# Optimization experiments

Measured on AMD Instinct MI355X. Metric: run time of the kernel, lower is better.

## Reference

```python
import jax, jax.numpy as jnp
import numpy as np

EPS = 1e-5  # torch.nn.LayerNorm default

def layernorm(x, gamma, beta):
    mu = jnp.mean(x, axis=-1, keepdims=True)
    var = jnp.mean(jnp.square(x - mu), axis=-1, keepdims=True)
    return (x - mu) * jax.lax.rsqrt(var + EPS) * gamma + beta

def setup_inputs() -> dict:
    key = jax.random.key(0)
    ks = jax.random.split(key, 5)
    B, H = 8192, 1024
    stdv = 1.0 / np.sqrt(H)
    inp = jax.random.normal(ks[0], (B, 4 * H), dtype=jnp.float32)
    hx = jax.random.normal(ks[1], (B, H), dtype=jnp.float32)
    cx = jax.random.normal(ks[2], (B, H), dtype=jnp.float32)
    weight_hh = jax.random.uniform(ks[3], (4 * H, H), dtype=jnp.float32, minval=-stdv, maxval=stdv)
    gamma_h = jnp.ones((4 * H,), jnp.float32)
    beta_h = jnp.zeros((4 * H,), jnp.float32)
    gamma_c = jnp.ones((H,), jnp.float32)
    beta_c = jnp.zeros((H,), jnp.float32)
    return {"input": inp, "hx": hx, "cx": cx, "weight_hh": weight_hh,
            "gamma_h": gamma_h, "beta_h": beta_h, "gamma_c": gamma_c, "beta_c": beta_c}

def reference(input, hx, cx, weight_hh, gamma_h, beta_h, gamma_c, beta_c):
    # hgates = LN(hx @ W_hh^T); gates = igates + hgates
    hgates = layernorm(jnp.matmul(hx, weight_hh.T), gamma_h, beta_h)
    gates = input + hgates  # [B, 4H]
    i_g, f_g, c_g, o_g = jnp.split(gates, 4, axis=1)
    ingate = jax.nn.sigmoid(i_g)
    forgetgate = jax.nn.sigmoid(f_g)
    cellgate = jnp.tanh(c_g)
    outgate = jax.nn.sigmoid(o_g)
    cy = layernorm(forgetgate * cx + ingate * cellgate, gamma_c, beta_c)
    hy = outgate * jnp.tanh(cy)
    return (hy, cy)
```

## Files before the change

### kernel.cpp

```cpp
#include <hip/hip_runtime.h>
#include <hip/hip_bf16.h>

typedef __attribute__((ext_vector_type(8))) short short8;
typedef __attribute__((ext_vector_type(4))) float f32x4;

#define LN_EPS 1e-5f

__device__ __forceinline__ ushort f32_to_bf16(float f) {
  union { float f; unsigned u; } v; v.f = f;
  unsigned u = v.u;
  u += 0x7FFFu + ((u >> 16) & 1u);
  return (ushort)(u >> 16);
}
__device__ __forceinline__ float bf16_to_f32(ushort h) {
  union { unsigned u; float f; } v; v.u = ((unsigned)h) << 16; return v.f;
}
__device__ __forceinline__ float sigmoid_f(float x) {
  return 1.0f / (1.0f + __expf(-x));
}
__device__ __forceinline__ float tanh_f(float x) {
  return 2.0f / (1.0f + __expf(-2.0f * x)) - 1.0f;
}

__global__ __launch_bounds__(256) void cast_f32_bf16(const float* __restrict__ in,
                                                     ushort* __restrict__ out, int n4) {
  int i = blockIdx.x * 256 + threadIdx.x;
  int stride = gridDim.x * 256;
  for (; i < n4; i += stride) {
    float4 v = ((const float4*)in)[i];
    ushort4 o;
    o.x = f32_to_bf16(v.x); o.y = f32_to_bf16(v.y);
    o.z = f32_to_bf16(v.z); o.w = f32_to_bf16(v.w);
    ((ushort4*)out)[i] = o;
  }
}

__global__ __launch_bounds__(256) void gemm_bt(const ushort* __restrict__ A,
                                               const ushort* __restrict__ B,
                                               ushort* __restrict__ C,
                                               int M, int N, int K) {
  __shared__ alignas(16) ushort As[128][40];
  __shared__ alignas(16) ushort Bs[128][40];
  const int tid = threadIdx.x;
  const int lane = tid & 63;
  const int wave = tid >> 6;
  const int wm = wave >> 1, wn = wave & 1;
  const int bn = blockIdx.x, bm = blockIdx.y;

  f32x4 acc[4][4];
#pragma unroll
  for (int i = 0; i < 4; i++)
#pragma unroll
    for (int j = 0; j < 4; j++) acc[i][j] = (f32x4){0.f, 0.f, 0.f, 0.f};

  const int srow = tid >> 2;
  const int scol = (tid & 3) << 3;
  const ushort* Ag = A + (size_t)(bm * 128 + srow) * K + scol;
  const ushort* Bg = B + (size_t)(bn * 128 + srow) * K + scol;
  const int frow = lane & 15;
  const int fcol = (lane >> 4) << 3;

  for (int k0 = 0; k0 < K; k0 += 32) {
    short8 a0 = *(const short8*)(Ag);
    short8 a1 = *(const short8*)(Ag + (size_t)64 * K);
    short8 b0 = *(const short8*)(Bg);
    short8 b1 = *(const short8*)(Bg + (size_t)64 * K);
    __syncthreads();
    *(short8*)&As[srow][scol]      = a0;
    *(short8*)&As[srow + 64][scol] = a1;
    *(short8*)&Bs[srow][scol]      = b0;
    *(short8*)&Bs[srow + 64][scol] = b1;
    __syncthreads();
    Ag += 32; Bg += 32;

    short8 af[4], bfr[4];
#pragma unroll
    for (int i = 0; i < 4; i++) af[i]  = *(const short8*)&As[wm * 64 + i * 16 + frow][fcol];
#pragma unroll
    for (int j = 0; j < 4; j++) bfr[j] = *(const short8*)&Bs[wn * 64 + j * 16 + frow][fcol];
#pragma unroll
    for (int i = 0; i < 4; i++)
#pragma unroll
      for (int j = 0; j < 4; j++)
        acc[i][j] = __builtin_amdgcn_mfma_f32_16x16x32_bf16(af[i], bfr[j], acc[i][j], 0, 0, 0);
  }

  const int crow0 = bm * 128 + wm * 64;
  const int ccol0 = bn * 128 + wn * 64;
#pragma unroll
  for (int i = 0; i < 4; i++)
#pragma unroll
    for (int j = 0; j < 4; j++) {
      int col = ccol0 + j * 16 + (lane & 15);
      int rb = crow0 + i * 16 + ((lane >> 4) << 2);
#pragma unroll
      for (int r = 0; r < 4; r++)
        C[(size_t)(rb + r) * N + col] = f32_to_bf16(acc[i][j][r]);
    }
}

__global__ __launch_bounds__(256) void lstm_ln_kernel(
    const ushort* __restrict__ gates_pre,
    const float* __restrict__ input,
    const float* __restrict__ cx,
    const float* __restrict__ gamma_h, const float* __restrict__ beta_h,
    const float* __restrict__ gamma_c, const float* __restrict__ beta_c,
    float* __restrict__ hy, float* __restrict__ cy, int H) {
  const int FH = 4 * H;
  const int row = blockIdx.x;
  const int t = threadIdx.x;
  const int lane = t & 63, wv = t >> 6;
  __shared__ float gates_s[4096];
  __shared__ float redA[8], redB[8];

  const ushort* gp = gates_pre + (size_t)row * FH;
  const int c0 = t * 8;
  const int c1 = 2048 + t * 8;

  float x[16];
  {
    uint4 u0 = *(const uint4*)(gp + c0);
    uint4 u1 = *(const uint4*)(gp + c1);
    const unsigned* pu0 = (const unsigned*)&u0;
    const unsigned* pu1 = (const unsigned*)&u1;
#pragma unroll
    for (int q = 0; q < 4; q++) {
      x[2 * q]     = bf16_to_f32((ushort)(pu0[q] & 0xFFFFu));
      x[2 * q + 1] = bf16_to_f32((ushort)(pu0[q] >> 16));
      x[8 + 2 * q]     = bf16_to_f32((ushort)(pu1[q] & 0xFFFFu));
      x[8 + 2 * q + 1] = bf16_to_f32((ushort)(pu1[q] >> 16));
    }
  }

  float s1 = 0.f, s2 = 0.f;
#pragma unroll
  for (int q = 0; q < 16; q++) { s1 += x[q]; s2 += x[q] * x[q]; }
  {
    float a = s1, b = s2;
#pragma unroll
    for (int off = 32; off > 0; off >>= 1) {
      a += __shfl_down(a, off, 64);
      b += __shfl_down(b, off, 64);
    }
    if (lane == 0) { redA[wv] = a; redA[4 + wv] = b; }
  }
  __syncthreads();
  const float mu  = (redA[0] + redA[1] + redA[2] + redA[3]) * (1.0f / 4096.f);
  const float m2  = (redA[4] + redA[5] + redA[6] + redA[7]) * (1.0f / 4096.f);
  const float rstd = rsqrtf(m2 - mu * mu + LN_EPS);

  const float* ip = input + (size_t)row * FH;
#pragma unroll
  for (int h = 0; h < 2; h++) {
    const int cc = (h == 0) ? c0 : c1;
    const int xo = h * 8;
    float iv[8], gv[8], bv[8];
    *(float4*)&iv[0] = *(const float4*)(ip + cc);
    *(float4*)&iv[4] = *(const float4*)(ip + cc + 4);
    *(float4*)&gv[0] = *(const float4*)(gamma_h + cc);
    *(float4*)&gv[4] = *(const float4*)(gamma_h + cc + 4);
    *(float4*)&bv[0] = *(const float4*)(beta_h + cc);
    *(float4*)&bv[4] = *(const float4*)(beta_h + cc + 4);
#pragma unroll
    for (int q = 0; q < 8; q++)
      gates_s[cc + q] = (x[xo + q] - mu) * rstd * gv[q] + bv[q] + iv[q];
  }
  __syncthreads();

  const float* cxp = cx + (size_t)row * H;
  float cell[4], og[4];
  float s3 = 0.f, s4 = 0.f;
#pragma unroll
  for (int k = 0; k < 4; k++) {
    const int j = t + 256 * k;
    float ig = gates_s[j];
    float fg = gates_s[H + j];
    float cg = gates_s[2 * H + j];
    float oo = gates_s[3 * H + j];
    float in_s = sigmoid_f(ig);
    float fg_s = sigmoid_f(fg);
    float cg_t = tanh_f(cg);
    og[k] = sigmoid_f(oo);
    float cl = fg_s * cxp[j] + in_s * cg_t;
    cell[k] = cl;
    s3 += cl; s4 += cl * cl;
  }
  {
    float a = s3, b = s4;
#pragma unroll
    for (int off = 32; off > 0; off >>= 1) {
      a += __shfl_down(a, off, 64);
      b += __shfl_down(b, off, 64);
    }
    if (lane == 0) { redB[wv] = a; redB[4 + wv] = b; }
  }
  __syncthreads();
  const float mu2   = (redB[0] + redB[1] + redB[2] + redB[3]) * (1.0f / 1024.f);
  const float m22   = (redB[4] + redB[5] + redB[6] + redB[7]) * (1.0f / 1024.f);
  const float rstd2 = rsqrtf(m22 - mu2 * mu2 + LN_EPS);

#pragma unroll
  for (int k = 0; k < 4; k++) {
    const int j = t + 256 * k;
    float cyv = (cell[k] - mu2) * rstd2 * gamma_c[j] + beta_c[j];
    float hyv = og[k] * tanh_f(cyv);
    cy[(size_t)row * H + j] = cyv;
    hy[(size_t)row * H + j] = hyv;
  }
}

extern "C" void kernel_launch(void* const* d_in, const int* in_sizes, int n_in,
                              void* d_out, int out_size, void* d_ws, size_t ws_size,
                              hipStream_t stream) {
  (void)n_in; (void)out_size; (void)ws_size;
  const float* input   = (const float*)d_in[0];
  const float* hx      = (const float*)d_in[1];
  const float* cx      = (const float*)d_in[2];
  const float* w       = (const float*)d_in[3];
  const float* gamma_h = (const float*)d_in[4];
  const float* beta_h  = (const float*)d_in[5];
  const float* gamma_c = (const float*)d_in[6];
  const float* beta_c  = (const float*)d_in[7];

  const int H  = in_sizes[6];
  const int B  = in_sizes[1] / H;
  const int FH = 4 * H;
  const int K  = H;

  ushort* hx_bf = (ushort*)d_ws;
  ushort* w_bf  = hx_bf + (size_t)B * K;
  ushort* gates = w_bf + (size_t)FH * K;

  float* hy = (float*)d_out;
  float* cy = hy + (size_t)B * H;

  cast_f32_bf16<<<2048, 256, 0, stream>>>(hx, hx_bf, (B * K) / 4);
  cast_f32_bf16<<<1024, 256, 0, stream>>>(w, w_bf, (FH * K) / 4);

  dim3 grid(FH / 128, B / 128);
  gemm_bt<<<grid, 256, 0, stream>>>(hx_bf, w_bf, gates, B, FH, K);

  lstm_ln_kernel<<<B, 256, 0, stream>>>(gates, input, cx, gamma_h, beta_h,
                                        gamma_c, beta_c, hy, cy, H);
}
```

Measured before the change: 382.5 us.

## Use direct global-to-LDS loads with XOR swizzle, merge casts, regularize LSTM epilogue

```diff
diff --git a/kernel.cpp b/kernel.cpp
--- a/kernel.cpp
+++ b/kernel.cpp
@@ -22,16 +22,26 @@
   return 2.0f / (1.0f + __expf(-2.0f * x)) - 1.0f;
 }
 
-__global__ __launch_bounds__(256) void cast_f32_bf16(const float* __restrict__ in,
-                                                     ushort* __restrict__ out, int n4) {
+__device__ __forceinline__ void gload16(const ushort* g, ushort* l) {
+  __builtin_amdgcn_global_load_lds(
+      (const __attribute__((address_space(1))) unsigned int*)g,
+      (__attribute__((address_space(3))) unsigned int*)l, 16, 0, 0);
+}
+
+__global__ __launch_bounds__(256) void cast2_f32_bf16(
+    const float* __restrict__ a, ushort* __restrict__ oa, int na4,
+    const float* __restrict__ b, ushort* __restrict__ ob, int nb4) {
   int i = blockIdx.x * 256 + threadIdx.x;
   int stride = gridDim.x * 256;
-  for (; i < n4; i += stride) {
-    float4 v = ((const float4*)in)[i];
+  for (; i < na4 + nb4; i += stride) {
+    const float* src = (i < na4) ? a : b;
+    ushort* dst = (i < na4) ? oa : ob;
+    int k = (i < na4) ? i : i - na4;
+    float4 v = ((const float4*)src)[k];
     ushort4 o;
     o.x = f32_to_bf16(v.x); o.y = f32_to_bf16(v.y);
     o.z = f32_to_bf16(v.z); o.w = f32_to_bf16(v.w);
-    ((ushort4*)out)[i] = o;
+    ((ushort4*)dst)[k] = o;
   }
 }
 
@@ -39,8 +49,8 @@
                                                const ushort* __restrict__ B,
                                                ushort* __restrict__ C,
                                                int M, int N, int K) {
-  __shared__ alignas(16) ushort As[128][40];
-  __shared__ alignas(16) ushort Bs[128][40];
+  __shared__ alignas(16) ushort As[128 * 32];
+  __shared__ alignas(16) ushort Bs[128 * 32];
   const int tid = threadIdx.x;
   const int lane = tid & 63;
   const int wave = tid >> 6;
@@ -54,30 +64,35 @@
     for (int j = 0; j < 4; j++) acc[i][j] = (f32x4){0.f, 0.f, 0.f, 0.f};
 
   const int srow = tid >> 2;
-  const int scol = (tid & 3) << 3;
-  const ushort* Ag = A + (size_t)(bm * 128 + srow) * K + scol;
-  const ushort* Bg = B + (size_t)(bn * 128 + srow) * K + scol;
+  const int schunk = (tid & 3) ^ ((tid >> 3) & 3);
+  const ushort* Ag = A + (size_t)(bm * 128 + srow) * K + schunk * 8;
+  const ushort* Bg = B + (size_t)(bn * 128 + srow) * K + schunk * 8;
+  ushort* Asl = As + tid * 8;
+  ushort* Bsl = Bs + tid * 8;
+  const size_t rowstep = (size_t)64 * K;
+
   const int frow = lane & 15;
-  const int fcol = (lane >> 4) << 3;
+  const int rchunk = (lane >> 4) ^ ((frow >> 1) & 3);
+  int aoff[4], boff[4];
+#pragma unroll
+  for (int i = 0; i < 4; i++) {
+    aoff[i] = (wm * 64 + i * 16 + frow) * 32 + rchunk * 8;
+    boff[i] = (wn * 64 + i * 16 + frow) * 32 + rchunk * 8;
+  }
 
   for (int k0 = 0; k0 < K; k0 += 32) {
-    short8 a0 = *(const short8*)(Ag);
-    short8 a1 = *(const short8*)(Ag + (size_t)64 * K);
-    short8 b0 = *(const short8*)(Bg);
-    short8 b1 = *(const short8*)(Bg + (size_t)64 * K);
     __syncthreads();
-    *(short8*)&As[srow][scol]      = a0;
-    *(short8*)&As[srow + 64][scol] = a1;
-    *(short8*)&Bs[srow][scol]      = b0;
-    *(short8*)&Bs[srow + 64][scol] = b1;
+    gload16(Ag + k0, Asl);
+    gload16(Ag + rowstep + k0, Asl + 2048);
+    gload16(Bg + k0, Bsl);
+    gload16(Bg + rowstep + k0, Bsl + 2048);
     __syncthreads();
-    Ag += 32; Bg += 32;
 
     short8 af[4], bfr[4];
 #pragma unroll
-    for (int i = 0; i < 4; i++) af[i]  = *(const short8*)&As[wm * 64 + i * 16 + frow][fcol];
-#pragma unroll
-    for (int j = 0; j < 4; j++) bfr[j] = *(const short8*)&Bs[wn * 64 + j * 16 + frow][fcol];
+    for (int i = 0; i < 4; i++) af[i]  = *(const short8*)&As[aoff[i]];
+#pragma unroll
+    for (int j = 0; j < 4; j++) bfr[j] = *(const short8*)&Bs[boff[j]];
 #pragma unroll
     for (int i = 0; i < 4; i++)
 #pragma unroll
@@ -110,31 +125,26 @@
   const int row = blockIdx.x;
   const int t = threadIdx.x;
   const int lane = t & 63, wv = t >> 6;
-  __shared__ float gates_s[4096];
+  const int j0 = t * 4;
   __shared__ float redA[8], redB[8];
 
   const ushort* gp = gates_pre + (size_t)row * FH;
-  const int c0 = t * 8;
-  const int c1 = 2048 + t * 8;
-
-  float x[16];
+
+  float xg[4][4];
   {
-    uint4 u0 = *(const uint4*)(gp + c0);
-    uint4 u1 = *(const uint4*)(gp + c1);
-    const unsigned* pu0 = (const unsigned*)&u0;
-    const unsigned* pu1 = (const unsigned*)&u1;
-#pragma unroll
-    for (int q = 0; q < 4; q++) {
-      x[2 * q]     = bf16_to_f32((ushort)(pu0[q] & 0xFFFFu));
-      x[2 * q + 1] = bf16_to_f32((ushort)(pu0[q] >> 16));
-      x[8 + 2 * q]     = bf16_to_f32((ushort)(pu1[q] & 0xFFFFu));
-      x[8 + 2 * q + 1] = bf16_to_f32((ushort)(pu1[q] >> 16));
+#pragma unroll
+    for (int g = 0; g < 4; g++) {
+      ushort4 u = *(const ushort4*)(gp + g * H + j0);
+      xg[g][0] = bf16_to_f32(u.x); xg[g][1] = bf16_to_f32(u.y);
+      xg[g][2] = bf16_to_f32(u.z); xg[g][3] = bf16_to_f32(u.w);
     }
   }
 
   float s1 = 0.f, s2 = 0.f;
 #pragma unroll
-  for (int q = 0; q < 16; q++) { s1 += x[q]; s2 += x[q] * x[q]; }
+  for (int g = 0; g < 4; g++)
+#pragma unroll
+    for (int q = 0; q < 4; q++) { s1 += xg[g][q]; s2 += xg[g][q] * xg[g][q]; }
   {
     float a = s1, b = s2;
 #pragma unroll
@@ -145,44 +155,36 @@
     if (lane == 0) { redA[wv] = a; redA[4 + wv] = b; }
   }
   __syncthreads();
-  const float mu  = (redA[0] + redA[1] + redA[2] + redA[3]) * (1.0f / 4096.f);
-  const float m2  = (redA[4] + redA[5] + redA[6] + redA[7]) * (1.0f / 4096.f);
+  const float inv_fh = 1.0f / (float)FH;
+  const float mu  = (redA[0] + redA[1] + redA[2] + redA[3]) * inv_fh;
+  const float m2  = (redA[4] + redA[5] + redA[6] + redA[7]) * inv_fh;
   const float rstd = rsqrtf(m2 - mu * mu + LN_EPS);
 
   const float* ip = input + (size_t)row * FH;
-#pragma unroll
-  for (int h = 0; h < 2; h++) {
-    const int cc = (h == 0) ? c0 : c1;
-    const int xo = h * 8;
-    float iv[8], gv[8], bv[8];
-    *(float4*)&iv[0] = *(const float4*)(ip + cc);
-    *(float4*)&iv[4] = *(const float4*)(ip + cc + 4);
-    *(float4*)&gv[0] = *(const float4*)(gamma_h + cc);
-    *(float4*)&gv[4] = *(const float4*)(gamma_h + cc + 4);
-    *(float4*)&bv[0] = *(const float4*)(beta_h + cc);
-    *(float4*)&bv[4] = *(const float4*)(beta_h + cc + 4);
-#pragma unroll
-    for (int q = 0; q < 8; q++)
-      gates_s[cc + q] = (x[xo + q] - mu) * rstd * gv[q] + bv[q] + iv[q];
-  }
-  __syncthreads();
-
-  const float* cxp = cx + (size_t)row * H;
+  float a_g[4][4];
+#pragma unroll
+  for (int g = 0; g < 4; g++) {
+    float4 iv = *(const float4*)(ip + g * H + j0);
+    float4 gv = *(const float4*)(gamma_h + g * H + j0);
+    float4 bv = *(const float4*)(beta_h + g * H + j0);
+    a_g[g][0] = (xg[g][0] - mu) * rstd * gv.x + bv.x + iv.x;
+    a_g[g][1] = (xg[g][1] - mu) * rstd * gv.y + bv.y + iv.y;
+    a_g[g][2] = (xg[g][2] - mu) * rstd * gv.z + bv.z + iv.z;
+    a_g[g][3] = (xg[g][3] - mu) * rstd * gv.w + bv.w + iv.w;
+  }
+
+  float4 cxv = *(const float4*)(cx + (size_t)row * H + j0);
+  const float* cxa = (const float*)&cxv;
   float cell[4], og[4];
   float s3 = 0.f, s4 = 0.f;
 #pragma unroll
-  for (int k = 0; k < 4; k++) {
-    const int j = t + 256 * k;
-    float ig = gates_s[j];
-    float fg = gates_s[H + j];
-    float cg = gates_s[2 * H + j];
-    float oo = gates_s[3 * H + j];
-    float in_s = sigmoid_f(ig);
-    float fg_s = sigmoid_f(fg);
-    float cg_t = tanh_f(cg);
-    og[k] = sigmoid_f(oo);
-    float cl = fg_s * cxp[j] + in_s * cg_t;
-    cell[k] = cl;
+  for (int q = 0; q < 4; q++) {
+    float in_s = sigmoid_f(a_g[0][q]);
+    float fg_s = sigmoid_f(a_g[1][q]);
+    float cg_t = tanh_f(a_g[2][q]);
+    og[q] = sigmoid_f(a_g[3][q]);
+    float cl = fg_s * cxa[q] + in_s * cg_t;
+    cell[q] = cl;
     s3 += cl; s4 += cl * cl;
   }
   {
@@ -195,18 +197,25 @@
     if (lane == 0) { redB[wv] = a; redB[4 + wv] = b; }
   }
   __syncthreads();
-  const float mu2   = (redB[0] + redB[1] + redB[2] + redB[3]) * (1.0f / 1024.f);
-  const float m22   = (redB[4] + redB[5] + redB[6] + redB[7]) * (1.0f / 1024.f);
+  const float inv_h = 1.0f / (float)H;
+  const float mu2   = (redB[0] + redB[1] + redB[2] + redB[3]) * inv_h;
+  const float m22   = (redB[4] + redB[5] + redB[6] + redB[7]) * inv_h;
   const float rstd2 = rsqrtf(m22 - mu2 * mu2 + LN_EPS);
 
-#pragma unroll
-  for (int k = 0; k < 4; k++) {
-    const int j = t + 256 * k;
-    float cyv = (cell[k] - mu2) * rstd2 * gamma_c[j] + beta_c[j];
-    float hyv = og[k] * tanh_f(cyv);
-    cy[(size_t)row * H + j] = cyv;
-    hy[(size_t)row * H + j] = hyv;
-  }
+  float4 gc = *(const float4*)(gamma_c + j0);
+  float4 bc = *(const float4*)(beta_c + j0);
+  const float* gca = (const float*)&gc;
+  const float* bca = (const float*)&bc;
+  float4 cyo, hyo;
+  float* cyp = (float*)&cyo; float* hyp = (float*)&hyo;
+#pragma unroll
+  for (int q = 0; q < 4; q++) {
+    float cyv = (cell[q] - mu2) * rstd2 * gca[q] + bca[q];
+    cyp[q] = cyv;
+    hyp[q] = og[q] * tanh_f(cyv);
+  }
+  *(float4*)(cy + (size_t)row * H + j0) = cyo;
+  *(float4*)(hy + (size_t)row * H + j0) = hyo;
 }
 
 extern "C" void kernel_launch(void* const* d_in, const int* in_sizes, int n_in,
@@ -234,8 +243,8 @@
   float* hy = (float*)d_out;
   float* cy = hy + (size_t)B * H;
 
-  cast_f32_bf16<<<2048, 256, 0, stream>>>(hx, hx_bf, (B * K) / 4);
-  cast_f32_bf16<<<1024, 256, 0, stream>>>(w, w_bf, (FH * K) / 4);
+  cast2_f32_bf16<<<2048, 256, 0, stream>>>(hx, hx_bf, (B * K) / 4,
+                                           w, w_bf, (FH * K) / 4);
 
   dim3 grid(FH / 128, B / 128);
   gemm_bt<<<grid, 256, 0, stream>>>(hx_bf, w_bf, gates, B, FH, K);
```

New measurement: 366.0 us. 4.3% less time.
